# Optimization experiments

Measured on AMD Instinct MI355X. Metric: run time of the kernel, lower is better.

Reference implementation:

```python
import jax, jax.numpy as jnp
import numpy as np
import math
from math import factorial

L = 3            # SH degree -> (L+1)^2 = 16 basis functions
H = 1024         # coefficient grid height
W = 1024         # coefficient grid width
B = 1048576      # number of rays (1024x1024 render)


def _norm_lm(l, m):
    return math.sqrt((2 * l + 1) / (4 * math.pi) * (factorial(l - m) / factorial(l + m)))


def real_spherical_harmonics(dirs, L):
    """dirs: [N,3] float32 -> [N,(L+1)^2] float32 real SH basis."""
    eps = 1e-14
    r = jnp.linalg.norm(dirs, axis=-1) + eps
    xd, yd, zd = dirs[:, 0], dirs[:, 1], dirs[:, 2]
    theta = jnp.arccos(jnp.clip(zd / r, -1.0, 1.0))
    phi = jnp.arctan2(yd, xd)
    ct = jnp.cos(theta)
    # Associated Legendre P_l^m(ct) via the standard recursion (loops over the
    # small fixed (l,m) set unroll at trace time; all ops vectorized over N).
    p = {(0, 0): jnp.ones_like(ct)}
    if L >= 1:
        p[(1, 0)] = ct
        s = jnp.sqrt(jnp.clip(1.0 - ct * ct, 1e-14, None))
        p[(1, 1)] = s
        for l in range(2, L + 1):
            p[(l, l)] = (2 * l - 1) * s * p[(l - 1, l - 1)]
            for m in range(l - 1, -1, -1):
                a = (2 * l - 1) * ct * p[(l - 1, m)]
                b = (l + m - 1) * p[(l - 2, m)] if (l - 2) >= m else 0.0
                p[(l, m)] = (a - b) / (l - m)
    cols = []
    sqrt2 = math.sqrt(2.0)
    for l in range(L + 1):
        for m in range(-l, l + 1):
            if m == 0:
                cols.append(_norm_lm(l, 0) * p[(l, 0)])
            elif m > 0:
                sign = (-1.0) ** m
                cols.append(sqrt2 * sign * _norm_lm(l, m) * p[(l, m)] * jnp.cos(m * phi))
            else:
                mp = -m
                sign = (-1.0) ** m
                cols.append(sqrt2 * sign * _norm_lm(l, mp) * p[(l, mp)] * jnp.sin(mp * phi))
    return jnp.stack(cols, axis=-1)  # [N, (L+1)^2]


def setup_inputs() -> dict:
    key = jax.random.key(0)
    k1, k2, k3, k4 = jax.random.split(key, 4)
    return {
        "y": jax.random.randint(k1, (B,), 0, H),
        "x": jax.random.randint(k2, (B,), 0, W),
        "ray_dir": jax.random.normal(k3, (B, 3), dtype=jnp.float32),
        "sh_data": 0.1 * jax.random.normal(k4, (H, W, (L + 1) ** 2, 3), dtype=jnp.float32),
    }


def reference(y, x, ray_dir, sh_data):
    coefs = sh_data[y, x]                       # [B, (L+1)^2, 3] gather
    B_mat = real_spherical_harmonics(ray_dir, L)  # [B, (L+1)^2]
    c = jnp.einsum('bi,bij->bj', B_mat, coefs)    # [B, 3]
    return jnp.clip(c, 0.0, 1.0)
```

## Files before the change

### kernel.cpp

```cpp
#include <hip/hip_runtime.h>


#define SH_C0   0.28209479177387814f
#define SH_C1   0.48860251190291992f
#define SH_C2a  1.09254843059207907f
#define SH_C2b  0.31539156525252005f
#define SH_C2c  0.54627421529603959f
#define SH_C3a  0.59004358992664352f
#define SH_C3b  2.89061144264055405f
#define SH_C3c  0.45704579946446572f
#define SH_C3d  0.37317633259011546f
#define SH_C3e  1.44530572132027702f

#define DO4(v, J0,C0, J1,C1, J2,C2, J3,C3)        \
    s##C0 = fmaf(b[J0], (v).x, s##C0);            \
    s##C1 = fmaf(b[J1], (v).y, s##C1);            \
    s##C2 = fmaf(b[J2], (v).z, s##C2);            \
    s##C3 = fmaf(b[J3], (v).w, s##C3);

__global__ __launch_bounds__(256) void sh_embed_coop(
    const int* __restrict__ ys, const int* __restrict__ xs,
    const float* __restrict__ dirs, const float* __restrict__ sh,
    float* __restrict__ out, int B)
{
    const int tid  = blockIdx.x * 256 + threadIdx.x;
    const int ray  = tid >> 2;
    const int q    = tid & 3;
    if (ray >= B) return;

    const int yy = ys[ray];
    const int xx = xs[ray];
    const float4* __restrict__ c4 =
        (const float4*)(sh + (size_t)(yy * 1024 + xx) * 48u);

    const float4 v0 = c4[q];
    const float4 v1 = c4[q + 4];
    const float4 v2 = c4[q + 8];

    const float dx = dirs[3 * ray + 0];
    const float dy = dirs[3 * ray + 1];
    const float dz = dirs[3 * ray + 2];
    const float inv = rsqrtf(fmaf(dx, dx, fmaf(dy, dy, dz * dz)));
    const float nx = dx * inv, ny = dy * inv, nz = dz * inv;

    const float x2 = nx * nx, y2 = ny * ny, z2 = nz * nz;
    const float xy = nx * ny, yz = ny * nz, xz = nx * nz;

    float b[16];
    b[0]  =  SH_C0;
    b[1]  = -SH_C1 * ny;
    b[2]  =  SH_C1 * nz;
    b[3]  = -SH_C1 * nx;
    b[4]  =  SH_C2a * xy;
    b[5]  = -SH_C2a * yz;
    b[6]  =  SH_C2b * (3.0f * z2 - 1.0f);
    b[7]  = -SH_C2a * xz;
    b[8]  =  SH_C2c * (x2 - y2);
    b[9]  = -SH_C3a * ny * (3.0f * x2 - y2);
    b[10] =  SH_C3b * xy * nz;
    b[11] = -SH_C3c * ny * (5.0f * z2 - 1.0f);
    b[12] =  SH_C3d * nz * (5.0f * z2 - 3.0f);
    b[13] = -SH_C3c * nx * (5.0f * z2 - 1.0f);
    b[14] =  SH_C3e * nz * (x2 - y2);
    b[15] = -SH_C3a * nx * (x2 - 3.0f * y2);

    float s0 = 0.0f, s1 = 0.0f, s2 = 0.0f;
    switch (q) {
    case 0:
        DO4(v0,  0,0,  0,1,  0,2,  1,0)
        DO4(v1,  5,1,  5,2,  6,0,  6,1)
        DO4(v2, 10,2, 11,0, 11,1, 11,2)
        break;
    case 1:
        DO4(v0,  1,1,  1,2,  2,0,  2,1)
        DO4(v1,  6,2,  7,0,  7,1,  7,2)
        DO4(v2, 12,0, 12,1, 12,2, 13,0)
        break;
    case 2:
        DO4(v0,  2,2,  3,0,  3,1,  3,2)
        DO4(v1,  8,0,  8,1,  8,2,  9,0)
        DO4(v2, 13,1, 13,2, 14,0, 14,1)
        break;
    default:
        DO4(v0,  4,0,  4,1,  4,2,  5,0)
        DO4(v1,  9,1,  9,2, 10,0, 10,1)
        DO4(v2, 14,2, 15,0, 15,1, 15,2)
        break;
    }

    s0 += __shfl_xor(s0, 1, 64);  s0 += __shfl_xor(s0, 2, 64);
    s1 += __shfl_xor(s1, 1, 64);  s1 += __shfl_xor(s1, 2, 64);
    s2 += __shfl_xor(s2, 1, 64);  s2 += __shfl_xor(s2, 2, 64);

    if (q < 3) {
        float val = (q == 0) ? s0 : (q == 1) ? s1 : s2;
        out[(size_t)3 * ray + q] = fminf(fmaxf(val, 0.0f), 1.0f);
    }
}

extern "C" void kernel_launch(void* const* d_in, const int* in_sizes, int n_in,
                              void* d_out, int out_size, void* d_ws, size_t ws_size,
                              hipStream_t stream) {
    const int*   ys   = (const int*)d_in[0];
    const int*   xs   = (const int*)d_in[1];
    const float* dirs = (const float*)d_in[2];
    const float* sh   = (const float*)d_in[3];
    float* out = (float*)d_out;
    int B = in_sizes[0];
    int blocks = (B + 63) / 64;
    sh_embed_coop<<<blocks, 256, 0, stream>>>(ys, xs, dirs, sh, out, B);
}
```

Measured before the change: 287.9 us.

## Bucket rays by row via counting sort before gathering SH coefficients

Adds a counting-sort pipeline: histogram of rays by y row, a scan for offsets, and an atomic scatter that writes direction and cell index into row-grouped records. The gather kernel then reads the coefficient table in row order, so nearby threads hit the same 192 KB row and the random 192-byte gathers get better cache locality. In exchange it adds four extra launches, atomics on 1024 hot counters, an extra round trip of 20 bytes per ray through workspace, and scattered final output writes.

```diff
diff --git a/kernel.cpp b/kernel.cpp
--- a/kernel.cpp
+++ b/kernel.cpp
@@ -1,5 +1,9 @@
 #include <hip/hip_runtime.h>
+#include <stdint.h>
 
+
+#define NB   1024
+#define PAD  16
 
 #define SH_C0   0.28209479177387814f
 #define SH_C1   0.48860251190291992f
@@ -18,33 +22,89 @@
     s##C2 = fmaf(b[J2], (v).z, s##C2);            \
     s##C3 = fmaf(b[J3], (v).w, s##C3);
 
-__global__ __launch_bounds__(256) void sh_embed_coop(
+__global__ __launch_bounds__(256) void zero_counts(uint32_t* __restrict__ counts, int n)
+{
+    int i = blockIdx.x * 256 + threadIdx.x;
+    if (i < n) counts[i] = 0u;
+}
+
+__global__ __launch_bounds__(256) void hist_kernel(
+    const int* __restrict__ ys, uint32_t* __restrict__ counts, int B)
+{
+    __shared__ uint32_t h[NB];
+    for (int i = threadIdx.x; i < NB; i += 256) h[i] = 0u;
+    __syncthreads();
+    int base = blockIdx.x * 4096 + threadIdx.x;
+#pragma unroll
+    for (int k = 0; k < 16; ++k) {
+        int r = base + k * 256;
+        if (r < B) atomicAdd(&h[ys[r]], 1u);
+    }
+    __syncthreads();
+    for (int i = threadIdx.x; i < NB; i += 256) {
+        uint32_t v = h[i];
+        if (v) atomicAdd(&counts[i * PAD], v);
+    }
+}
+
+__global__ __launch_bounds__(1024) void scan_kernel(
+    const uint32_t* __restrict__ counts, uint32_t* __restrict__ cursors)
+{
+    __shared__ uint32_t t[NB];
+    int i = threadIdx.x;
+    uint32_t v = counts[i * PAD];
+    t[i] = v;
+    __syncthreads();
+    for (int off = 1; off < NB; off <<= 1) {
+        uint32_t add = (i >= off) ? t[i - off] : 0u;
+        __syncthreads();
+        t[i] += add;
+        __syncthreads();
+    }
+    cursors[i * PAD] = t[i] - v;
+}
+
+__global__ __launch_bounds__(256) void scatter_kernel(
     const int* __restrict__ ys, const int* __restrict__ xs,
-    const float* __restrict__ dirs, const float* __restrict__ sh,
-    float* __restrict__ out, int B)
+    const float* __restrict__ dirs, uint32_t* __restrict__ cursors,
+    float4* __restrict__ rec, int* __restrict__ rayid, int B)
 {
-    const int tid  = blockIdx.x * 256 + threadIdx.x;
-    const int ray  = tid >> 2;
-    const int q    = tid & 3;
-    if (ray >= B) return;
+    int r = blockIdx.x * 256 + threadIdx.x;
+    if (r >= B) return;
+    int yy = ys[r], xx = xs[r];
+    uint32_t pos = atomicAdd(&cursors[yy * PAD], 1u);
+    float dx = dirs[3 * r + 0];
+    float dy = dirs[3 * r + 1];
+    float dz = dirs[3 * r + 2];
+    int cell = yy * 1024 + xx;
+    rec[pos]   = make_float4(dx, dy, dz, __int_as_float(cell));
+    rayid[pos] = r;
+}
 
-    const int yy = ys[ray];
-    const int xx = xs[ray];
-    const float4* __restrict__ c4 =
-        (const float4*)(sh + (size_t)(yy * 1024 + xx) * 48u);
+__global__ __launch_bounds__(256) void gather_kernel(
+    const float4* __restrict__ rec, const int* __restrict__ rayid,
+    const float* __restrict__ sh, float* __restrict__ out, int B)
+{
+    int tid  = blockIdx.x * 256 + threadIdx.x;
+    int slot = tid >> 2;
+    int q    = tid & 3;
+    if (slot >= B) return;
 
-    const float4 v0 = c4[q];
-    const float4 v1 = c4[q + 4];
-    const float4 v2 = c4[q + 8];
+    float4 rc = rec[slot];
+    int cell  = __float_as_int(rc.w);
+    int ray   = rayid[slot];
+    const float4* __restrict__ c4 = (const float4*)(sh + (size_t)cell * 48u);
 
-    const float dx = dirs[3 * ray + 0];
-    const float dy = dirs[3 * ray + 1];
-    const float dz = dirs[3 * ray + 2];
-    const float inv = rsqrtf(fmaf(dx, dx, fmaf(dy, dy, dz * dz)));
-    const float nx = dx * inv, ny = dy * inv, nz = dz * inv;
+    float4 v0 = c4[q];
+    float4 v1 = c4[q + 4];
+    float4 v2 = c4[q + 8];
 
-    const float x2 = nx * nx, y2 = ny * ny, z2 = nz * nz;
-    const float xy = nx * ny, yz = ny * nz, xz = nx * nz;
+    float nxr = rc.x, nyr = rc.y, nzr = rc.z;
+    float inv = rsqrtf(fmaf(nxr, nxr, fmaf(nyr, nyr, nzr * nzr)));
+    float nx = nxr * inv, ny = nyr * inv, nz = nzr * inv;
+
+    float x2 = nx * nx, y2 = ny * ny, z2 = nz * nz;
+    float xy = nx * ny, yz = ny * nz, xz = nx * nz;
 
     float b[16];
     b[0]  =  SH_C0;
@@ -107,6 +167,17 @@
     const float* sh   = (const float*)d_in[3];
     float* out = (float*)d_out;
     int B = in_sizes[0];
-    int blocks = (B + 63) / 64;
-    sh_embed_coop<<<blocks, 256, 0, stream>>>(ys, xs, dirs, sh, out, B);
+
+    uint8_t* ws = (uint8_t*)d_ws;
+    uint32_t* counts  = (uint32_t*)(ws);
+    uint32_t* cursors = (uint32_t*)(ws + 65536);
+    float4*   rec     = (float4*)  (ws + 131072);
+    int*      rayid   = (int*)     (ws + 131072 + (size_t)16 * B);
+
+    zero_counts<<<(NB * PAD + 255) / 256, 256, 0, stream>>>(counts, NB * PAD);
+    hist_kernel<<<(B + 4095) / 4096, 256, 0, stream>>>(ys, counts, B);
+    scan_kernel<<<1, 1024, 0, stream>>>(counts, cursors);
+    scatter_kernel<<<(B + 255) / 256, 256, 0, stream>>>(ys, xs, dirs, cursors,
+                                                        rec, rayid, B);
+    gather_kernel<<<((B * 4) + 255) / 256, 256, 0, stream>>>(rec, rayid, sh, out, B);
 }
```

Measured after the change: 375.1 us. +30.3%, slower.

## Prefetch SH table into cache with warm kernel and use nontemporal streams

Applied to the files above, without the earlier changes.

Adds a pre-pass kernel that streams the whole 192MB SH coefficient table with coalesced reads, so the random gather in the main kernel hits in the large last-level cache instead of DRAM. Streaming inputs (indices, directions) and the output use nontemporal loads and stores so they do not evict the table. The pre-pass reads the full table every call, adding bandwidth cost, and it only helps if the table fits in cache. It also writes to the workspace buffer without checking ws_size.

```diff
diff --git a/kernel.cpp b/kernel.cpp
--- a/kernel.cpp
+++ b/kernel.cpp
@@ -1,4 +1,5 @@
 #include <hip/hip_runtime.h>
+#include <stdint.h>
 
 
 #define SH_C0   0.28209479177387814f
@@ -18,6 +19,19 @@
     s##C2 = fmaf(b[J2], (v).z, s##C2);            \
     s##C3 = fmaf(b[J3], (v).w, s##C3);
 
+__global__ __launch_bounds__(256) void warm_kernel(
+    const float4* __restrict__ t, float* __restrict__ sink, int n4)
+{
+    int tid    = blockIdx.x * 256 + threadIdx.x;
+    int stride = gridDim.x * 256;
+    float acc = 0.0f;
+    for (int i = tid; i < n4; i += stride) {
+        float4 v = t[i];
+        acc += v.x + v.y + v.z + v.w;
+    }
+    __builtin_nontemporal_store(acc, sink + tid);
+}
+
 __global__ __launch_bounds__(256) void sh_embed_coop(
     const int* __restrict__ ys, const int* __restrict__ xs,
     const float* __restrict__ dirs, const float* __restrict__ sh,
@@ -28,8 +42,8 @@
     const int q    = tid & 3;
     if (ray >= B) return;
 
-    const int yy = ys[ray];
-    const int xx = xs[ray];
+    const int yy = __builtin_nontemporal_load(ys + ray);
+    const int xx = __builtin_nontemporal_load(xs + ray);
     const float4* __restrict__ c4 =
         (const float4*)(sh + (size_t)(yy * 1024 + xx) * 48u);
 
@@ -37,9 +51,9 @@
     const float4 v1 = c4[q + 4];
     const float4 v2 = c4[q + 8];
 
-    const float dx = dirs[3 * ray + 0];
-    const float dy = dirs[3 * ray + 1];
-    const float dz = dirs[3 * ray + 2];
+    const float dx = __builtin_nontemporal_load(dirs + 3 * ray + 0);
+    const float dy = __builtin_nontemporal_load(dirs + 3 * ray + 1);
+    const float dz = __builtin_nontemporal_load(dirs + 3 * ray + 2);
     const float inv = rsqrtf(fmaf(dx, dx, fmaf(dy, dy, dz * dz)));
     const float nx = dx * inv, ny = dy * inv, nz = dz * inv;
 
@@ -94,7 +108,8 @@
 
     if (q < 3) {
         float val = (q == 0) ? s0 : (q == 1) ? s1 : s2;
-        out[(size_t)3 * ray + q] = fminf(fmaxf(val, 0.0f), 1.0f);
+        val = fminf(fmaxf(val, 0.0f), 1.0f);
+        __builtin_nontemporal_store(val, out + (size_t)3 * ray + q);
     }
 }
 
@@ -107,6 +122,12 @@
     const float* sh   = (const float*)d_in[3];
     float* out = (float*)d_out;
     int B = in_sizes[0];
+
+    const int n4 = in_sizes[3] / 4;
+    const int warm_threads = 3072 * 256;
+    warm_kernel<<<3072, 256, 0, stream>>>((const float4*)sh, (float*)d_ws, n4);
+
     int blocks = (B + 63) / 64;
     sh_embed_coop<<<blocks, 256, 0, stream>>>(ys, xs, dirs, sh, out, B);
+    (void)warm_threads; (void)ws_size; (void)out_size; (void)n_in;
 }
```

Result: slower. 322.2 us (+11.9%).
